# Kernel optimization log

Measured on AMD Instinct MI355X. Metric: run time of the kernel, lower is better.

The kernel has to match this reference:

```python
import jax, jax.numpy as jnp
import numpy as np

B, S, D = 2, 2048, 2048
H, KV, HD = 8, 2, 256
EPS = 1e-6
WINDOW = 512
ROPE_THETA = 1000000.0
NEG = -1e9


def setup_inputs() -> dict:
    key = jax.random.key(0)
    ks = jax.random.split(key, 6)
    hidden_states = jax.random.normal(ks[0], (B, S, D), dtype=jnp.float32)
    # rotary tables: [S, HD//2] freqs tiled to [B, S, HD]
    inv_freq = 1.0 / (ROPE_THETA ** (np.arange(0, HD, 2, dtype=np.float32) / HD))
    pos = np.arange(S, dtype=np.float32)
    freqs = np.outer(pos, inv_freq)                      # [S, HD/2]
    emb = np.concatenate([freqs, freqs], axis=-1)        # [S, HD]
    cos = jnp.broadcast_to(jnp.asarray(np.cos(emb))[None], (B, S, HD))
    sin = jnp.broadcast_to(jnp.asarray(np.sin(emb))[None], (B, S, HD))
    # causal sliding-window additive mask: allow k<=q and q-k < WINDOW
    q_idx = np.arange(S)[:, None]
    k_idx = np.arange(S)[None, :]
    allowed = (k_idx <= q_idx) & (q_idx - k_idx < WINDOW)
    attention_mask = jnp.asarray(np.where(allowed, 0.0, NEG).astype(np.float32))[None, None]
    sc = 0.02
    wq = jax.random.normal(ks[1], (D, H * HD), dtype=jnp.float32) * sc
    wk = jax.random.normal(ks[2], (D, KV * HD), dtype=jnp.float32) * sc
    wv = jax.random.normal(ks[3], (D, KV * HD), dtype=jnp.float32) * sc
    wo = jax.random.normal(ks[4], (H * HD, D), dtype=jnp.float32) * sc
    q_norm_w = jnp.ones((HD,), dtype=jnp.float32)
    k_norm_w = jnp.ones((HD,), dtype=jnp.float32)
    return dict(hidden_states=hidden_states, cos=cos, sin=sin,
                attention_mask=attention_mask, wq=wq, wk=wk, wv=wv, wo=wo,
                q_norm_w=q_norm_w, k_norm_w=k_norm_w)


def _rms_norm(x, w):
    xf = x.astype(jnp.float32)
    y = xf * jax.lax.rsqrt(jnp.mean(xf * xf, axis=-1, keepdims=True) + EPS)
    return (y * w).astype(x.dtype)


def _apply_rope(x, cos, sin):
    # x: [B, S, N, HD]; cos/sin: [B, S, HD] -> unsqueeze at dim 2
    c = cos[:, :, None, :]
    s = sin[:, :, None, :]
    x1, x2 = jnp.split(x, 2, axis=-1)
    rot = jnp.concatenate([-x2, x1], axis=-1)
    return x * c + rot * s


def reference(hidden_states, cos, sin, attention_mask, wq, wk, wv, wo,
              q_norm_w, k_norm_w):
    b, s, _ = hidden_states.shape
    n_rep = H // KV
    q = (hidden_states @ wq).reshape(b, s, H, HD)
    q = _apply_rope(_rms_norm(q, q_norm_w), cos, sin).transpose(0, 2, 1, 3)   # [B,H,S,HD]
    k = (hidden_states @ wk).reshape(b, s, KV, HD)
    k = _apply_rope(_rms_norm(k, k_norm_w), cos, sin).transpose(0, 2, 1, 3)   # [B,KV,S,HD]
    v = (hidden_states @ wv).reshape(b, s, KV, HD)
    v = _rms_norm(v, jnp.float32(1.0)).transpose(0, 2, 1, 3)                  # [B,KV,S,HD]
    k = jnp.repeat(k, n_rep, axis=1)  # GQA repeat_kv -> [B,H,S,HD]
    v = jnp.repeat(v, n_rep, axis=1)
    # Gemma3n uses scaling = 1.0 (QK-RMSNorm replaces 1/sqrt(d))
    scores = jnp.einsum('bhqd,bhkd->bhqk', q, k) + attention_mask[:, :, :, :s]
    probs = jax.nn.softmax(scores.astype(jnp.float32), axis=-1).astype(q.dtype)
    out = jnp.einsum('bhqk,bhkd->bhqd', probs, v)
    out = out.transpose(0, 2, 1, 3).reshape(b, s, H * HD)
    return out @ wo
```

## Files before the change

kernel.cpp:

```cpp
#include <hip/hip_runtime.h>
#include <hip/hip_bf16.h>
#include <hip/hip_fp16.h>
#include <type_traits>

#define B_ 2
#define S_ 2048
#define D_ 2048
#define H_ 8
#define KV_ 2
#define HD_ 256
#define WINDOW_ 512
#define EPS_ 1e-6f
#define MASKV_ -30000.0f

typedef _Float16 f16;
typedef _Float16 half8 __attribute__((ext_vector_type(8)));
typedef _Float16 half2v __attribute__((ext_vector_type(2)));
typedef _Float16 half4v __attribute__((ext_vector_type(4)));
typedef float floatx4 __attribute__((ext_vector_type(4)));
typedef float floatx8 __attribute__((ext_vector_type(8)));
typedef float floatx16 __attribute__((ext_vector_type(16)));

#define GLOAD_LDS16(g, l)                                                        \
    __builtin_amdgcn_global_load_lds(                                            \
        (const __attribute__((address_space(1))) unsigned int*)(g),              \
        (__attribute__((address_space(3))) unsigned int*)(l), 16, 0, 0)

#define VMWAIT(n) asm volatile("s_waitcnt vmcnt(" #n ")" ::: "memory")
#define IC(n) std::integral_constant<int, n>{}

__global__ __launch_bounds__(256) void prep(const float* __restrict__ x,
                                            const float* __restrict__ wq,
                                            const float* __restrict__ wk,
                                            const float* __restrict__ wv,
                                            const float* __restrict__ wo,
                                            f16* __restrict__ xh,
                                            f16* __restrict__ BT,
                                            f16* __restrict__ woT) {
    int bid = blockIdx.x;
    const int t = threadIdx.x;
    if (bid < 8192) {
        const int i = bid * 256 + t;
        float4 v = ((const float4*)x)[i];
        half4v hv = {(f16)v.x, (f16)v.y, (f16)v.z, (f16)v.w};
        ((half4v*)xh)[i] = hv;
        return;
    }
    bid -= 8192;
    const float* src;
    f16* dst;
    int C, bx, by;
    if (bid < 1024) {
        src = wq; dst = BT; C = 2048; bx = bid & 31; by = bid >> 5;
    } else if (bid < 1280) {
        const int b3 = bid - 1024;
        src = wk; dst = BT + (size_t)2048 * 2048; C = 512; bx = b3 & 7; by = b3 >> 3;
    } else if (bid < 1536) {
        const int b3 = bid - 1280;
        src = wv; dst = BT + (size_t)2560 * 2048; C = 512; bx = b3 & 7; by = b3 >> 3;
    } else {
        const int b3 = bid - 1536;
        src = wo; dst = woT; C = 2048; bx = b3 & 31; by = b3 >> 5;
    }
    __shared__ float tl[64][65];
    const int c0 = bx * 64, r0 = by * 64;
#pragma unroll
    for (int i = 0; i < 4; ++i) {
        const int idx = i * 256 + t;
        const int row = idx >> 4;
        const int c4 = (idx & 15) * 4;
        float4 v = *(const float4*)&src[(size_t)(r0 + row) * C + c0 + c4];
        tl[row][c4 + 0] = v.x; tl[row][c4 + 1] = v.y;
        tl[row][c4 + 2] = v.z; tl[row][c4 + 3] = v.w;
    }
    __syncthreads();
#pragma unroll
    for (int i = 0; i < 4; ++i) {
        const int idx = i * 256 + t;
        const int c = idx >> 4;
        const int r4 = (idx & 15) * 4;
        half4v hv = {(f16)tl[r4 + 0][c], (f16)tl[r4 + 1][c],
                     (f16)tl[r4 + 2][c], (f16)tl[r4 + 3][c]};
        *(half4v*)&dst[(size_t)(c0 + c) * 2048 + r0 + r4] = hv;
    }
}

#define CH_ 528
template <typename OutT>
__global__ __launch_bounds__(256) void gemm_f16(const f16* __restrict__ A,
                                                const f16* __restrict__ BT,
                                                OutT* __restrict__ C,
                                                int M, int N, int K) {
    __shared__ __align__(16) f16 sA[16 * CH_];
    __shared__ __align__(16) f16 sB[16 * CH_];

    const int t = threadIdx.x;
    const int lane = t & 63;
    const int w = t >> 6;
    const int l31 = lane & 31, q1 = lane >> 5;
    const int m0 = blockIdx.y * 128, n0 = blockIdx.x * 128;
    const int mw = (w & 1) * 64, nw = (w >> 1) * 64;

    floatx16 acc[4];
#pragma unroll
    for (int i = 0; i < 4; ++i) acc[i] = (floatx16)(0.f);

    const int r8 = lane >> 3;
    const int g = (lane & 7) ^ r8;

    for (int k0 = 0; k0 < K; k0 += 64) {
#pragma unroll
        for (int cc = 0; cc < 4; ++cc) {
            const int chunk = w * 4 + cc;
            const int row = chunk * 8 + r8;
            GLOAD_LDS16(A + (size_t)(m0 + row) * K + k0 + g * 8,
                        sA + chunk * CH_ + lane * 8);
            GLOAD_LDS16(BT + (size_t)(n0 + row) * K + k0 + g * 8,
                        sB + chunk * CH_ + lane * 8);
        }
        __syncthreads();

#pragma unroll
        for (int ks = 0; ks < 4; ++ks) {
            const int G = ks * 2 + q1;
            half8 af[2], bf[2];
#pragma unroll
            for (int mt = 0; mt < 2; ++mt) {
                const int ra = mw + mt * 32 + l31;
                af[mt] = *(const half8*)(sA + (ra >> 3) * CH_ + (ra & 7) * 64 +
                                         (G ^ (ra & 7)) * 8);
                const int rb = nw + mt * 32 + l31;
                bf[mt] = *(const half8*)(sB + (rb >> 3) * CH_ + (rb & 7) * 64 +
                                         (G ^ (rb & 7)) * 8);
            }
#pragma unroll
            for (int mt = 0; mt < 2; ++mt)
#pragma unroll
                for (int nt = 0; nt < 2; ++nt)
                    acc[mt * 2 + nt] = __builtin_amdgcn_mfma_f32_32x32x16_f16(
                        af[mt], bf[nt], acc[mt * 2 + nt], 0, 0, 0);
        }
        __syncthreads();
    }

#pragma unroll
    for (int mt = 0; mt < 2; ++mt)
#pragma unroll
        for (int nt = 0; nt < 2; ++nt)
#pragma unroll
            for (int r = 0; r < 16; ++r) {
                const int row = m0 + mw + mt * 32 + (r & 3) + 8 * (r >> 2) + 4 * q1;
                const int col = n0 + nw + nt * 32 + l31;
                C[(size_t)row * N + col] = (OutT)acc[mt * 2 + nt][r];
            }
}

template <typename OutT>
__global__ __launch_bounds__(512, 2) void gemm_8p(const f16* __restrict__ A,
                                                  const f16* __restrict__ BT,
                                                  OutT* __restrict__ C,
                                                  int M, int N, int K) {
    __shared__ __align__(16) f16 sAA[4 * 8192];
    __shared__ __align__(16) f16 sBB[4 * 8192];

    const int tid = threadIdx.x;
    const int lane = tid & 63, w = tid >> 6;
    const int i16 = lane & 15, q4 = lane >> 4;
    const int w1 = w & 1, w2 = w >> 1;
    const int m0 = blockIdx.y * 256, n0 = blockIdx.x * 256;

    const int srow0 = tid >> 3;
    const int kx = ((tid & 7) ^ ((tid >> 3) & 7)) * 8;
    const f16* srcA0 = A + (size_t)(m0 + srow0) * K;
    const f16* srcB0 = BT + (size_t)(n0 + srow0) * K;
    f16* dstA0 = sAA + tid * 8;
    f16* dstB0 = sBB + tid * 8;

    auto stage = [&](int P, int kt) {
        const int half = P >> 1;
        const int slot = (2 * kt + half) & 3;
        const int kb = kt * 64 + kx;
        if ((P & 1) == 0) {
            const f16* s = srcA0 + (size_t)(half * 128) * K + kb;
            f16* d = dstA0 + slot * 8192;
            GLOAD_LDS16(s, d);
            GLOAD_LDS16(s + (size_t)64 * K, d + 4096);
        } else {
            const f16* s = srcB0 + (size_t)(half * 128) * K + kb;
            f16* d = dstB0 + slot * 8192;
            GLOAD_LDS16(s, d);
            GLOAD_LDS16(s + (size_t)64 * K, d + 4096);
        }
    };

    const int arow = (w1 * 64 + i16) * 64;
    const int brow = (w2 * 32 + i16) * 64;
    int xk[2];
    xk[0] = ((0 + q4) ^ (i16 & 7)) * 8;
    xk[1] = ((4 + q4) ^ (i16 & 7)) * 8;

    floatx4 acc[4][4][2];
#pragma unroll
    for (int p = 0; p < 4; ++p)
#pragma unroll
        for (int mt = 0; mt < 4; ++mt)
#pragma unroll
            for (int nt = 0; nt < 2; ++nt)
                acc[p][mt][nt] = (floatx4){0.f, 0.f, 0.f, 0.f};

    int st = 0;

    auto phase = [&](auto Pc, bool dostage, int ktn) {
        constexpr int P = decltype(Pc)::value;
        constexpr int qm = P & 1, qn = P >> 1;
        __builtin_amdgcn_s_barrier();
        const f16* ab = sAA + (size_t)(st + qm) * 8192;
        const f16* bb = sBB + (size_t)(st + qn) * 8192;
        half8 af[4][2], bf[2][2];
#pragma unroll
        for (int mt = 0; mt < 4; ++mt)
#pragma unroll
            for (int ks = 0; ks < 2; ++ks)
                af[mt][ks] = *(const half8*)(ab + arow + mt * 1024 + xk[ks]);
#pragma unroll
        for (int nt = 0; nt < 2; ++nt)
#pragma unroll
            for (int ks = 0; ks < 2; ++ks)
                bf[nt][ks] = *(const half8*)(bb + brow + nt * 1024 + xk[ks]);
        if (dostage) stage(P, ktn);
        __builtin_amdgcn_s_setprio(1);
#pragma unroll
        for (int mt = 0; mt < 4; ++mt)
#pragma unroll
            for (int nt = 0; nt < 2; ++nt)
#pragma unroll
                for (int ks = 0; ks < 2; ++ks)
                    acc[P][mt][nt] = __builtin_amdgcn_mfma_f32_16x16x32_f16(
                        af[mt][ks], bf[nt][ks], acc[P][mt][nt], 0, 0, 0);
        __builtin_amdgcn_s_setprio(0);
    };

    const int NT = K >> 6;

    stage(0, 0); stage(1, 0); stage(2, 0); stage(3, 0);

    for (int T = 0; T < NT - 1; ++T) {
        VMWAIT(4); phase(IC(0), true, T + 1);
        VMWAIT(4); phase(IC(1), true, T + 1);
        VMWAIT(4); phase(IC(2), true, T + 1);
        phase(IC(3), true, T + 1);
        st ^= 2;
    }
    VMWAIT(4); phase(IC(0), false, 0);
    VMWAIT(2); phase(IC(1), false, 0);
    VMWAIT(0); phase(IC(2), false, 0);
    phase(IC(3), false, 0);

#pragma unroll
    for (int p = 0; p < 4; ++p) {
        const int rb = m0 + (p & 1) * 128 + w1 * 64 + q4 * 4;
        const int cb = n0 + (p >> 1) * 128 + w2 * 32 + i16;
#pragma unroll
        for (int mt = 0; mt < 4; ++mt)
#pragma unroll
            for (int nt = 0; nt < 2; ++nt) {
                floatx4 v = acc[p][mt][nt];
#pragma unroll
                for (int r = 0; r < 4; ++r)
                    C[(size_t)(rb + mt * 16 + r) * N + cb + nt * 16] = (OutT)v[r];
            }
    }
}

#define NRBK_ ((B_ * S_ * KV_) / 4)

__global__ __launch_bounds__(256) void norm_kv_f16(
    const f16* __restrict__ QKVh, f16* __restrict__ Kh, f16* __restrict__ Vt,
    const float* __restrict__ cosb, const float* __restrict__ sinb,
    const float* __restrict__ kw) {
    __shared__ f16 vt[64][266];

    const int w = threadIdx.x >> 6, lane = threadIdx.x & 63;

    if (blockIdx.x < NRBK_) {
        const int wid = blockIdx.x * 4 + w;
        const int d0 = lane * 2;
        const int b = wid / (S_ * KV_);
        const int r = wid % (S_ * KV_);
        const int s = r / KV_, kv = r % KV_;
        const f16* p = QKVh + (size_t)(b * S_ + s) * 3072 + 2048 + kv * HD_;
        half2v lo = *(const half2v*)(p + d0);
        half2v hi = *(const half2v*)(p + 128 + d0);
        float x0 = (float)lo[0], x1 = (float)lo[1], x2 = (float)hi[0], x3 = (float)hi[1];
        float ss = x0 * x0 + x1 * x1 + x2 * x2 + x3 * x3;
#pragma unroll
        for (int off = 32; off >= 1; off >>= 1) ss += __shfl_xor(ss, off);
        const float inv = rsqrtf(ss * (1.0f / HD_) + EPS_);
        float2 wlo = *(const float2*)(kw + d0), whi = *(const float2*)(kw + 128 + d0);
        float y0 = x0 * inv * wlo.x, y1 = x1 * inv * wlo.y;
        float y2 = x2 * inv * whi.x, y3 = x3 * inv * whi.y;
        const float* cb = cosb + (size_t)(b * S_ + s) * HD_;
        const float* sb = sinb + (size_t)(b * S_ + s) * HD_;
        float2 clo = *(const float2*)(cb + d0), chi = *(const float2*)(cb + 128 + d0);
        float2 slo = *(const float2*)(sb + d0), shi = *(const float2*)(sb + 128 + d0);
        half2v olo = {(f16)(y0 * clo.x - y2 * slo.x), (f16)(y1 * clo.y - y3 * slo.y)};
        half2v ohi = {(f16)(y2 * chi.x + y0 * shi.x), (f16)(y3 * chi.y + y1 * shi.y)};
        f16* d = Kh + ((size_t)(b * KV_ + kv) * S_ + s) * HD_;
        *(half2v*)(d + d0) = olo;
        *(half2v*)(d + 128 + d0) = ohi;
        return;
    }

    const int vb = blockIdx.x - NRBK_;
    const int s0 = (vb & 31) * 64;
    const int kv = (vb >> 5) & 1;
    const int b  = vb >> 6;

    for (int r = 0; r < 16; ++r) {
        const int sl = w * 16 + r;
        const f16* p = QKVh + (size_t)(b * S_ + s0 + sl) * 3072 + 2560 + kv * HD_;
        const int d0 = lane * 2;
        half2v lo = *(const half2v*)(p + d0);
        half2v hi = *(const half2v*)(p + 128 + d0);
        float x0 = (float)lo[0], x1 = (float)lo[1], x2 = (float)hi[0], x3 = (float)hi[1];
        float ss = x0 * x0 + x1 * x1 + x2 * x2 + x3 * x3;
#pragma unroll
        for (int off = 32; off >= 1; off >>= 1) ss += __shfl_xor(ss, off);
        const float inv = rsqrtf(ss * (1.0f / HD_) + EPS_);
        half2v olo = {(f16)(x0 * inv), (f16)(x1 * inv)};
        half2v ohi = {(f16)(x2 * inv), (f16)(x3 * inv)};
        *(half2v*)&vt[sl][d0] = olo;
        *(half2v*)&vt[sl][128 + d0] = ohi;
    }
    __syncthreads();
    f16* dst = Vt + (size_t)(b * KV_ + kv) * HD_ * S_;
    for (int i = 0; i < 64; ++i) {
        const int dd = w * 64 + i;
        dst[(size_t)dd * S_ + s0 + lane] = vt[lane][dd];
    }
}

__global__ __launch_bounds__(512, 2) void attn_mfma(const f16* __restrict__ QKVh,
                                                    const f16* __restrict__ Kh,
                                                    const f16* __restrict__ Vt,
                                                    f16* __restrict__ attnh,
                                                    const float* __restrict__ cosb,
                                                    const float* __restrict__ sinb,
                                                    const float* __restrict__ qw) {
    __shared__ __align__(16) f16 sK[2][64 * 256];
    __shared__ __align__(16) f16 sV[2][256 * 64];
    __shared__ __align__(16) f16 sP[8][16 * 72];

    const int qt = blockIdx.x, h = blockIdx.y, b = blockIdx.z;
    const int kvh = h / (H_ / KV_);
    const int t = threadIdx.x, lane = t & 63, w = t >> 6;
    const int i16 = lane & 15, q4 = lane >> 4;

    const int qrow = qt * 128 + w * 16 + i16;
    const f16* qbase = QKVh + (size_t)(b * S_ + qrow) * 3072 + h * HD_ + q4 * 8;
    half8 qf[8];
#pragma unroll
    for (int kk = 0; kk < 8; ++kk) qf[kk] = *(const half8*)(qbase + kk * 32);

    {
        float ss = 0.f;
#pragma unroll
        for (int kk = 0; kk < 8; ++kk)
#pragma unroll
            for (int j = 0; j < 8; ++j) {
                const float v = (float)qf[kk][j];
                ss += v * v;
            }
        ss += __shfl_xor(ss, 16);
        ss += __shfl_xor(ss, 32);
        const float inv = rsqrtf(ss * (1.0f / HD_) + EPS_);
        const float* cb = cosb + (size_t)(b * S_ + qrow) * HD_ + q4 * 8;
        const float* sb = sinb + (size_t)(b * S_ + qrow) * HD_ + q4 * 8;
        const float* wp = qw + q4 * 8;
#pragma unroll
        for (int kk = 0; kk < 4; ++kk) {
            const int dl = kk * 32, dh = dl + 128;
            floatx8 cl = *(const floatx8*)(cb + dl);
            floatx8 ch = *(const floatx8*)(cb + dh);
            floatx8 sl = *(const floatx8*)(sb + dl);
            floatx8 sh = *(const floatx8*)(sb + dh);
            floatx8 wl = *(const floatx8*)(wp + dl);
            floatx8 wh = *(const floatx8*)(wp + dh);
            half8 nl, nh;
#pragma unroll
            for (int j = 0; j < 8; ++j) {
                const float xl = (float)qf[kk][j] * inv * wl[j];
                const float xh = (float)qf[kk + 4][j] * inv * wh[j];
                nl[j] = (f16)(xl * cl[j] - xh * sl[j]);
                nh[j] = (f16)(xh * ch[j] + xl * sh[j]);
            }
            qf[kk] = nl;
            qf[kk + 4] = nh;
        }
    }

    floatx4 o[16];
#pragma unroll
    for (int i = 0; i < 16; ++i) o[i] = (floatx4){0.f, 0.f, 0.f, 0.f};
    float mrow[4] = {-1e30f, -1e30f, -1e30f, -1e30f};
    float lrow[4] = {0.f, 0.f, 0.f, 0.f};

    const size_t kbase = (size_t)(b * KV_ + kvh) * S_ * HD_;
    const size_t vbase = (size_t)(b * KV_ + kvh) * HD_ * S_;
    const int srow0 = qt * 128 + w * 16 + q4 * 4;

    const int kt_lo = (2 * qt - 8) > 0 ? (2 * qt - 8) : 0;
    const int kt_hi = 2 * qt + 1;
    const int s_lo_w = qt * 128 + w * 16;
    int ktw_lo = (s_lo_w - (WINDOW_ - 1)) >> 6;
    if (ktw_lo < kt_lo) ktw_lo = kt_lo;
    const int ktw_hi = (s_lo_w + 15) >> 6;

    auto stage = [&](int kt, int buf) {
#pragma unroll
        for (int c = 0; c < 4; ++c) {
            const int chunk = w * 4 + c;
            const int keyl = chunk * 2 + (lane >> 5);
            const int g = (lane & 31) ^ (keyl & 31);
            GLOAD_LDS16(Kh + kbase + (size_t)(kt * 64 + keyl) * HD_ + g * 8,
                        sK[buf] + chunk * 512 + lane * 8);
            const int diml = chunk * 8 + (lane >> 3);
            const int g2 = (lane & 7) ^ (diml & 7);
            GLOAD_LDS16(Vt + vbase + (size_t)diml * S_ + kt * 64 + g2 * 8,
                        sV[buf] + chunk * 512 + lane * 8);
        }
    };

    stage(kt_lo, 0);
    int cur = 0;
    for (int kt = kt_lo; kt <= kt_hi; ++kt, cur ^= 1) {
        __syncthreads();
        if (kt < kt_hi) stage(kt + 1, cur ^ 1);
        if (kt < ktw_lo || kt > ktw_hi) continue;

        const f16* sKc = sK[cur];
        const f16* sVc = sV[cur];

        floatx4 sc[4];
#pragma unroll
        for (int nt = 0; nt < 4; ++nt) sc[nt] = (floatx4){0.f, 0.f, 0.f, 0.f};
#pragma unroll
        for (int ks = 0; ks < 8; ++ks)
#pragma unroll
            for (int nt = 0; nt < 4; ++nt) {
                const int keyl = nt * 16 + i16;
                const int gp = (ks * 4 + q4) ^ (keyl & 31);
                half8 kf = *(const half8*)(sKc + keyl * 256 + gp * 8);
                sc[nt] = __builtin_amdgcn_mfma_f32_16x16x32_f16(qf[ks], kf, sc[nt], 0, 0, 0);
            }

#pragma unroll
        for (int r = 0; r < 4; ++r) {
            const int s = srow0 + r;
            float mx = -1e30f;
#pragma unroll
            for (int nt = 0; nt < 4; ++nt) {
                const int j = kt * 64 + nt * 16 + i16;
                const bool valid = (j <= s) && (s - j < WINDOW_);
                const float v = valid ? sc[nt][r] : MASKV_;
                sc[nt][r] = v;
                mx = fmaxf(mx, v);
            }
#pragma unroll
            for (int off = 1; off < 16; off <<= 1) mx = fmaxf(mx, __shfl_xor(mx, off));
            const float mnew = fmaxf(mrow[r], mx);
            const float alpha = __expf(mrow[r] - mnew);
            mrow[r] = mnew;
            float rs = 0.f;
#pragma unroll
            for (int nt = 0; nt < 4; ++nt) {
                const float p = __expf(sc[nt][r] - mnew);
                sc[nt][r] = p;
                rs += p;
            }
#pragma unroll
            for (int off = 1; off < 16; off <<= 1) rs += __shfl_xor(rs, off);
            lrow[r] = lrow[r] * alpha + rs;
#pragma unroll
            for (int nt2 = 0; nt2 < 16; ++nt2) o[nt2][r] *= alpha;
        }

        f16* sPw = sP[w];
#pragma unroll
        for (int nt = 0; nt < 4; ++nt)
#pragma unroll
            for (int r = 0; r < 4; ++r)
                sPw[(q4 * 4 + r) * 72 + nt * 16 + i16] = (f16)sc[nt][r];
        asm volatile("s_waitcnt lgkmcnt(0)" ::: "memory");

#pragma unroll
        for (int kt2 = 0; kt2 < 2; ++kt2) {
            half8 pf = *(const half8*)(sPw + i16 * 72 + kt2 * 32 + q4 * 8);
#pragma unroll
            for (int nt2 = 0; nt2 < 16; ++nt2) {
                const int dim = nt2 * 16 + i16;
                const int gp = (kt2 * 4 + q4) ^ (dim & 7);
                half8 vf = *(const half8*)(sVc + dim * 64 + gp * 8);
                o[nt2] = __builtin_amdgcn_mfma_f32_16x16x32_f16(pf, vf, o[nt2], 0, 0, 0);
            }
        }
    }

    float inv2[4];
#pragma unroll
    for (int r = 0; r < 4; ++r) inv2[r] = 1.0f / lrow[r];
    f16* ob = attnh + (size_t)(b * S_ + qt * 128 + w * 16) * (H_ * HD_) + h * HD_;
#pragma unroll
    for (int nt2 = 0; nt2 < 16; ++nt2)
#pragma unroll
        for (int r = 0; r < 4; ++r)
            ob[(size_t)(q4 * 4 + r) * (H_ * HD_) + nt2 * 16 + i16] =
                (f16)(o[nt2][r] * inv2[r]);
}

extern "C" void kernel_launch(void* const* d_in, const int* in_sizes, int n_in,
                              void* d_out, int out_size, void* d_ws, size_t ws_size,
                              hipStream_t stream) {
    const float* x    = (const float*)d_in[0];
    const float* cosb = (const float*)d_in[1];
    const float* sinb = (const float*)d_in[2];
    const float* wq = (const float*)d_in[4];
    const float* wk = (const float*)d_in[5];
    const float* wv = (const float*)d_in[6];
    const float* wo = (const float*)d_in[7];
    const float* qw = (const float*)d_in[8];
    const float* kw = (const float*)d_in[9];
    float* out = (float*)d_out;

    f16* ws = (f16*)d_ws;
    f16* xh    = ws;
    f16* BT    = xh + 8388608;
    f16* woT   = BT + 6291456;
    f16* QKVh  = woT + 4194304;
    f16* Kh    = QKVh + 12582912;
    f16* Vt    = Kh + 2097152;
    f16* attnh = xh;

    const int M = B_ * S_;

    prep<<<8192 + 2560, 256, 0, stream>>>(x, wq, wk, wv, wo, xh, BT, woT);

    gemm_8p<f16><<<dim3(12, 16), 512, 0, stream>>>(xh, BT, QKVh, M, 3072, D_);

    norm_kv_f16<<<NRBK_ + 128, 256, 0, stream>>>(QKVh, Kh, Vt, cosb, sinb, kw);

    attn_mfma<<<dim3(S_ / 128, H_, B_), 512, 0, stream>>>(QKVh, Kh, Vt, attnh,
                                                          cosb, sinb, qw);

    gemm_f16<float><<<dim3(16, 32), 256, 0, stream>>>(attnh, woT, out, M, D_, H_ * HD_);
}
```

Before: 313.7 us.

## Reorder 8-phase GEMM quadrants to reuse register fragments across phases

Restructures the 256x256 GEMM mainloop so quadrants are visited in a snake order (A0B0, A0B1, A1B1, A1B0). Each phase now reloads only the A or the B fragment instead of both, cutting LDS reads. Stage order, vmcnt waits and barriers are rearranged to match, with explicit lgkmcnt waits and extra barriers around each MFMA block. The additional barriers per phase may add synchronization cost that offsets the saved LDS traffic.

```diff
diff --git a/kernel.cpp b/kernel.cpp
--- a/kernel.cpp
+++ b/kernel.cpp
@@ -27,7 +27,7 @@
         (__attribute__((address_space(3))) unsigned int*)(l), 16, 0, 0)
 
 #define VMWAIT(n) asm volatile("s_waitcnt vmcnt(" #n ")" ::: "memory")
-#define IC(n) std::integral_constant<int, n>{}
+#define LGKM0 asm volatile("s_waitcnt lgkmcnt(0)" ::: "memory")
 
 __global__ __launch_bounds__(256) void prep(const float* __restrict__ x,
                                             const float* __restrict__ wq,
@@ -169,28 +169,25 @@
     const int w1 = w & 1, w2 = w >> 1;
     const int m0 = blockIdx.y * 256, n0 = blockIdx.x * 256;
 
-    const int srow0 = tid >> 3;
     const int kx = ((tid & 7) ^ ((tid >> 3) & 7)) * 8;
-    const f16* srcA0 = A + (size_t)(m0 + srow0) * K;
-    const f16* srcB0 = BT + (size_t)(n0 + srow0) * K;
+    const f16* srcA0 = A + (size_t)(m0 + (tid >> 3)) * K;
+    const f16* srcB0 = BT + (size_t)(n0 + (tid >> 3)) * K;
     f16* dstA0 = sAA + tid * 8;
     f16* dstB0 = sBB + tid * 8;
 
-    auto stage = [&](int P, int kt) {
-        const int half = P >> 1;
+    auto stageA = [&](int half, int kt) {
         const int slot = (2 * kt + half) & 3;
-        const int kb = kt * 64 + kx;
-        if ((P & 1) == 0) {
-            const f16* s = srcA0 + (size_t)(half * 128) * K + kb;
-            f16* d = dstA0 + slot * 8192;
-            GLOAD_LDS16(s, d);
-            GLOAD_LDS16(s + (size_t)64 * K, d + 4096);
-        } else {
-            const f16* s = srcB0 + (size_t)(half * 128) * K + kb;
-            f16* d = dstB0 + slot * 8192;
-            GLOAD_LDS16(s, d);
-            GLOAD_LDS16(s + (size_t)64 * K, d + 4096);
-        }
+        const f16* s = srcA0 + (size_t)(half * 128) * K + kt * 64 + kx;
+        f16* d = dstA0 + slot * 8192;
+        GLOAD_LDS16(s, d);
+        GLOAD_LDS16(s + (size_t)64 * K, d + 4096);
+    };
+    auto stageB = [&](int half, int kt) {
+        const int slot = (2 * kt + half) & 3;
+        const f16* s = srcB0 + (size_t)(half * 128) * K + kt * 64 + kx;
+        f16* d = dstB0 + slot * 8192;
+        GLOAD_LDS16(s, d);
+        GLOAD_LDS16(s + (size_t)64 * K, d + 4096);
     };
 
     const int arow = (w1 * 64 + i16) * 64;
@@ -210,56 +207,86 @@
 
     int st = 0;
 
-    auto phase = [&](auto Pc, bool dostage, int ktn) {
-        constexpr int P = decltype(Pc)::value;
-        constexpr int qm = P & 1, qn = P >> 1;
-        __builtin_amdgcn_s_barrier();
-        const f16* ab = sAA + (size_t)(st + qm) * 8192;
-        const f16* bb = sBB + (size_t)(st + qn) * 8192;
-        half8 af[4][2], bf[2][2];
-#pragma unroll
-        for (int mt = 0; mt < 4; ++mt)
-#pragma unroll
-            for (int ks = 0; ks < 2; ++ks)
-                af[mt][ks] = *(const half8*)(ab + arow + mt * 1024 + xk[ks]);
-#pragma unroll
-        for (int nt = 0; nt < 2; ++nt)
-#pragma unroll
-            for (int ks = 0; ks < 2; ++ks)
-                bf[nt][ks] = *(const half8*)(bb + brow + nt * 1024 + xk[ks]);
-        if (dostage) stage(P, ktn);
-        __builtin_amdgcn_s_setprio(1);
-#pragma unroll
-        for (int mt = 0; mt < 4; ++mt)
-#pragma unroll
-            for (int nt = 0; nt < 2; ++nt)
-#pragma unroll
-                for (int ks = 0; ks < 2; ++ks)
-                    acc[P][mt][nt] = __builtin_amdgcn_mfma_f32_16x16x32_f16(
-                        af[mt][ks], bf[nt][ks], acc[P][mt][nt], 0, 0, 0);
-        __builtin_amdgcn_s_setprio(0);
+    const int NT = K >> 6;
+
+    stageA(0, 0); stageB(0, 0); stageB(1, 0); stageA(1, 0);
+    VMWAIT(4);
+    __builtin_amdgcn_s_barrier();
+
+    half8 af[4][2], bf[2][2];
+
+#define READ_A(ptr)                                                           \
+    _Pragma("unroll") for (int mt = 0; mt < 4; ++mt)                          \
+        _Pragma("unroll") for (int ks = 0; ks < 2; ++ks)                      \
+            af[mt][ks] = *(const half8*)((ptr) + arow + mt * 1024 + xk[ks]);
+#define READ_B(ptr)                                                           \
+    _Pragma("unroll") for (int nt = 0; nt < 2; ++nt)                          \
+        _Pragma("unroll") for (int ks = 0; ks < 2; ++ks)                      \
+            bf[nt][ks] = *(const half8*)((ptr) + brow + nt * 1024 + xk[ks]);
+#define DO_MFMA(p)                                                            \
+    __builtin_amdgcn_s_setprio(1);                                            \
+    _Pragma("unroll") for (int mt = 0; mt < 4; ++mt)                          \
+        _Pragma("unroll") for (int nt = 0; nt < 2; ++nt)                      \
+            _Pragma("unroll") for (int ks = 0; ks < 2; ++ks)                  \
+                acc[p][mt][nt] = __builtin_amdgcn_mfma_f32_16x16x32_f16(      \
+                    af[mt][ks], bf[nt][ks], acc[p][mt][nt], 0, 0, 0);         \
+    __builtin_amdgcn_s_setprio(0);
+
+    auto tile = [&](auto LASTC, int T) {
+        constexpr bool LAST = decltype(LASTC)::value;
+        const f16* a0p = sAA + (size_t)(st + 0) * 8192;
+        const f16* a1p = sAA + (size_t)(st + 1) * 8192;
+        const f16* b0p = sBB + (size_t)(st + 0) * 8192;
+        const f16* b1p = sBB + (size_t)(st + 1) * 8192;
+
+        READ_A(a0p); READ_B(b0p);
+        if constexpr (!LAST) stageA(0, T + 1);
+        __builtin_amdgcn_s_barrier();
+        LGKM0;
+        DO_MFMA(0);
+        if constexpr (!LAST) VMWAIT(4); else VMWAIT(2);
+        __builtin_amdgcn_s_barrier();
+
+        READ_B(b1p);
+        if constexpr (!LAST) stageB(0, T + 1);
+        __builtin_amdgcn_s_barrier();
+        LGKM0;
+        DO_MFMA(1);
+        if constexpr (!LAST) VMWAIT(4); else VMWAIT(0);
+        __builtin_amdgcn_s_barrier();
+
+        READ_A(a1p);
+        if constexpr (!LAST) stageB(1, T + 1);
+        __builtin_amdgcn_s_barrier();
+        LGKM0;
+        DO_MFMA(2);
+        __builtin_amdgcn_s_barrier();
+
+        READ_B(b0p);
+        if constexpr (!LAST) stageA(1, T + 1);
+        __builtin_amdgcn_s_barrier();
+        LGKM0;
+        DO_MFMA(3);
+        if constexpr (!LAST) { VMWAIT(4); }
+        __builtin_amdgcn_s_barrier();
     };
 
-    const int NT = K >> 6;
-
-    stage(0, 0); stage(1, 0); stage(2, 0); stage(3, 0);
-
     for (int T = 0; T < NT - 1; ++T) {
-        VMWAIT(4); phase(IC(0), true, T + 1);
-        VMWAIT(4); phase(IC(1), true, T + 1);
-        VMWAIT(4); phase(IC(2), true, T + 1);
-        phase(IC(3), true, T + 1);
+        tile(std::false_type{}, T);
         st ^= 2;
     }
-    VMWAIT(4); phase(IC(0), false, 0);
-    VMWAIT(2); phase(IC(1), false, 0);
-    VMWAIT(0); phase(IC(2), false, 0);
-    phase(IC(3), false, 0);
-
+    tile(std::true_type{}, NT - 1);
+
+#undef READ_A
+#undef READ_B
+#undef DO_MFMA
+
+    const int qmv[4] = {0, 0, 1, 1};
+    const int qnv[4] = {0, 1, 1, 0};
 #pragma unroll
     for (int p = 0; p < 4; ++p) {
-        const int rb = m0 + (p & 1) * 128 + w1 * 64 + q4 * 4;
-        const int cb = n0 + (p >> 1) * 128 + w2 * 32 + i16;
+        const int rb = m0 + qmv[p] * 128 + w1 * 64 + q4 * 4;
+        const int cb = n0 + qnv[p] * 128 + w2 * 32 + i16;
 #pragma unroll
         for (int mt = 0; mt < 4; ++mt)
 #pragma unroll
```

Result: no change. 311.8 us (-0.6%).
